# Performance work log

Hardware: AMD Instinct MI355X
Metric: run time of the kernel (lower is better)

The kernel has to match this reference:

```python
import jax, jax.numpy as jnp
import numpy as np

SEQ = 8192
EMB = 1024
MID = 1024


def setup_inputs() -> dict:
    key = jax.random.key(0)
    ks = jax.random.split(key, 7)
    s = 1.0 / np.sqrt(EMB)
    return {
        "text_encoded": jax.random.normal(ks[0], (SEQ, EMB), dtype=jnp.float32),
        "Wq": jax.random.normal(ks[1], (MID, EMB), dtype=jnp.float32) * s,
        "bq": jax.random.normal(ks[2], (MID,), dtype=jnp.float32) * 0.02,
        "Wk": jax.random.normal(ks[3], (MID, EMB), dtype=jnp.float32) * s,
        "bk": jax.random.normal(ks[4], (MID,), dtype=jnp.float32) * 0.02,
        "Wv": jax.random.normal(ks[5], (MID, EMB), dtype=jnp.float32) * s,
        "bv": jax.random.normal(ks[6], (MID,), dtype=jnp.float32) * 0.02,
    }


def reference(text_encoded, Wq, bq, Wk, bk, Wv, bv):
    # torch nn.Linear: y = x @ W.T + b, W is [out, in]
    Q = text_encoded @ Wq.T + bq  # [S, M]
    K = text_encoded @ Wk.T + bk  # [S, M]
    V = text_encoded @ Wv.T + bv  # [S, M]
    # cosine-similarity scores: (Q K^T) scaled by outer(1/||Q||, 1/||K||)
    inv_qn = jax.lax.rsqrt(jnp.sum(Q * Q, axis=1))  # [S]
    inv_kn = jax.lax.rsqrt(jnp.sum(K * K, axis=1))  # [S]
    scores = (Q @ K.T) * (inv_qn[:, None] * inv_kn[None, :])  # [S, S]
    weights = jax.nn.softmax(scores, axis=1)
    return weights @ V  # [S, M]
```

## Files before the change

### kernel.cpp

```cpp
#include <hip/hip_runtime.h>


#define SEQ 8192
#define MID 1024
#define EMB 1024

typedef __attribute__((ext_vector_type(8))) short short8x;
typedef __attribute__((ext_vector_type(16))) float float16x;
typedef __attribute__((ext_vector_type(4))) int int4x;
typedef __attribute__((ext_vector_type(16))) int int16x;

__device__ __forceinline__ unsigned short f2bf(float x) {
  union { float f; unsigned u; } v; v.f = x;
  unsigned r = v.u + 0x7FFFu + ((v.u >> 16) & 1u);
  return (unsigned short)(r >> 16);
}
__device__ __forceinline__ float bf2f(unsigned short h) {
  union { unsigned u; float f; } v; v.u = ((unsigned)h) << 16;
  return v.f;
}

__device__ __forceinline__ void g2l16(const void* g, void* lds) {
  __builtin_amdgcn_global_load_lds(
      (const __attribute__((address_space(1))) unsigned int*)g,
      (__attribute__((address_space(3))) unsigned int*)lds, 16, 0, 0);
}

__device__ __forceinline__ void gemm128_nt(
    const unsigned short* __restrict__ A, const unsigned short* __restrict__ B,
    long lda, long ldb, int m0, int n0, int K,
    unsigned short* As, unsigned short* Bs, float16x acc[2][2]) {
  const int tid = threadIdx.x;
  const int w = tid >> 6;
  const int l = tid & 63;
  const int wm = (w & 1) << 6;
  const int wn = (w >> 1) << 6;
  const int srow = l >> 3;
  const int skg = (l & 7) ^ srow;
  const int l31 = l & 31;
  const int lh = l >> 5;
  const int swz = l31 & 7;

  for (int k0 = 0; k0 < K; k0 += 64) {
    __syncthreads();
#pragma unroll
    for (int r = 0; r < 4; ++r) {
      const int rr = (w * 4 + r) * 8 + srow;
      g2l16(A + (long)(m0 + rr) * lda + k0 + skg * 8, As + (w * 4 + r) * 512);
      g2l16(B + (long)(n0 + rr) * ldb + k0 + skg * 8, Bs + (w * 4 + r) * 512);
    }
    __syncthreads();
#pragma unroll
    for (int ks = 0; ks < 4; ++ks) {
      const int kg = ks * 2 + lh;
      short8x av[2], bv[2];
#pragma unroll
      for (int t = 0; t < 2; ++t) {
        av[t] = *(const short8x*)(As + (wm + t * 32 + l31) * 64 + ((kg ^ swz) << 3));
        bv[t] = *(const short8x*)(Bs + (wn + t * 32 + l31) * 64 + ((kg ^ swz) << 3));
      }
#pragma unroll
      for (int tm = 0; tm < 2; ++tm)
#pragma unroll
        for (int tn = 0; tn < 2; ++tn)
          acc[tm][tn] = __builtin_amdgcn_mfma_f32_32x32x16_bf16(av[tm], bv[tn], acc[tm][tn], 0, 0, 0);
    }
  }
}

__device__ __forceinline__ void gemm128_nt_i8(
    const unsigned char* __restrict__ A, const unsigned char* __restrict__ B,
    long lda, long ldb, int m0, int n0, int Kbytes,
    unsigned char* As, unsigned char* Bs, int16x acc[2][2]) {
  const int tid = threadIdx.x;
  const int w = tid >> 6;
  const int l = tid & 63;
  const int wm = (w & 1) << 6;
  const int wn = (w >> 1) << 6;
  const int srow = l >> 3;
  const int skg = (l & 7) ^ srow;
  const int l31 = l & 31;
  const int lh = l >> 5;
  const int swz = l31 & 7;

  for (int k0 = 0; k0 < Kbytes; k0 += 128) {
    __syncthreads();
#pragma unroll
    for (int r = 0; r < 4; ++r) {
      const int rr = (w * 4 + r) * 8 + srow;
      g2l16(A + (long)(m0 + rr) * lda + k0 + skg * 16, As + (w * 4 + r) * 1024);
      g2l16(B + (long)(n0 + rr) * ldb + k0 + skg * 16, Bs + (w * 4 + r) * 1024);
    }
    __syncthreads();
#pragma unroll
    for (int ks = 0; ks < 4; ++ks) {
      const int kg = ks * 2 + lh;
      int4x av[2], bv[2];
#pragma unroll
      for (int t = 0; t < 2; ++t) {
        av[t] = *(const int4x*)(As + (wm + t * 32 + l31) * 128 + ((kg ^ swz) << 4));
        bv[t] = *(const int4x*)(Bs + (wn + t * 32 + l31) * 128 + ((kg ^ swz) << 4));
      }
#pragma unroll
      for (int tm = 0; tm < 2; ++tm)
#pragma unroll
        for (int tn = 0; tn < 2; ++tn)
          acc[tm][tn] = __builtin_amdgcn_mfma_i32_32x32x32_i8(av[tm], bv[tn], acc[tm][tn], 0, 0, 0);
    }
  }
}

__global__ void cvt_all(const float* __restrict__ X,
                        const float* __restrict__ wq, const float* __restrict__ wk,
                        const float* __restrict__ wv,
                        unsigned short* __restrict__ Xb, unsigned short* __restrict__ Wb,
                        float* __restrict__ sums) {
  const long i = ((long)blockIdx.x * 256 + threadIdx.x) * 4;
  if (i < 24576) *(float4*)(sums + i) = (float4){0.f, 0.f, 0.f, 0.f};
  const float* src;
  unsigned short* dst;
  long off;
  if (i < (long)SEQ * EMB) {
    src = X; dst = Xb; off = i;
  } else {
    long j = i - (long)SEQ * EMB;
    int t = (int)(j >> 20);
    off = j & (MID * EMB - 1);
    src = (t == 0) ? wq : (t == 1) ? wk : wv;
    dst = Wb + (long)t * MID * EMB;
  }
  float4 v = *(const float4*)(src + off);
  ushort4 o;
  o.x = f2bf(v.x); o.y = f2bf(v.y); o.z = f2bf(v.z); o.w = f2bf(v.w);
  *(ushort4*)(dst + off) = o;
}

__global__ __launch_bounds__(256) void qkv_kernel(
    const unsigned short* __restrict__ Xb, const unsigned short* __restrict__ Wb,
    const float* __restrict__ bq, const float* __restrict__ bk, const float* __restrict__ bv,
    unsigned char* __restrict__ Q8, unsigned char* __restrict__ K8,
    unsigned char* __restrict__ VT8, float* __restrict__ sumsq) {
  __shared__ unsigned short smem[16384];
  unsigned short* As = smem;
  unsigned short* Bs = smem + 8192;
  const int z = blockIdx.z;
  const int m0 = blockIdx.y * 128;
  const int n0 = blockIdx.x * 128;
  float16x acc[2][2];
#pragma unroll
  for (int i = 0; i < 2; ++i)
#pragma unroll
    for (int j = 0; j < 2; ++j)
#pragma unroll
      for (int e = 0; e < 16; ++e) acc[i][j][e] = 0.f;

  gemm128_nt(Xb, Wb + (long)z * MID * EMB, EMB, EMB, m0, n0, EMB, As, Bs, acc);

  const int tid = threadIdx.x;
  const int l = tid & 63, w = tid >> 6;
  const int wm = (w & 1) << 6, wn = (w >> 1) << 6;
  const int l31 = l & 31, lh = l >> 5;
  const float* bias = (z == 0) ? bq : (z == 1) ? bk : bv;
  float bvv[2];
#pragma unroll
  for (int tn = 0; tn < 2; ++tn) bvv[tn] = bias[n0 + wn + tn * 32 + l31];
#pragma unroll
  for (int tm = 0; tm < 2; ++tm)
#pragma unroll
    for (int tn = 0; tn < 2; ++tn)
#pragma unroll
      for (int r = 0; r < 16; ++r) acc[tm][tn][r] += bvv[tn];

  __syncthreads();

  if (z < 2) {
#pragma unroll
    for (int tm = 0; tm < 2; ++tm)
#pragma unroll
      for (int tn = 0; tn < 2; ++tn) {
        const int rcol = wn + tn * 32 + l31;
#pragma unroll
        for (int r = 0; r < 16; ++r) {
          float v = acc[tm][tn][r];
          float po = __shfl_xor(v, 1);
          if (!(l & 1)) {
            const int rrow = wm + tm * 32 + (r & 3) + 8 * (r >> 2) + 4 * lh;
            const int chunk = (rcol >> 3) ^ (rrow & 7);
            unsigned pk = (unsigned)f2bf(v) | ((unsigned)f2bf(po) << 16);
            *(unsigned*)(smem + rrow * 128 + (chunk << 3) + (rcol & 7)) = pk;
          }
        }
      }
    __syncthreads();
    unsigned char* O8 = z ? K8 : Q8;
    float* ss = sumsq + (long)z * SEQ;
    const float qs = 127.0f / 8.0f;
#pragma unroll
    for (int round = 0; round < 8; ++round) {
      const int row = round * 16 + (tid >> 4);
      const int c = tid & 15;
      short8x vv = *(const short8x*)(smem + row * 128 + ((c ^ (row & 7)) << 3));
      int qq[8];
      float s = 0.f;
#pragma unroll
      for (int j = 0; j < 8; ++j) {
        float t = rintf(bf2f((unsigned short)vv[j]) * qs);
        t = fminf(127.f, fmaxf(-127.f, t));
        qq[j] = (int)t;
        s += t * t;
      }
      unsigned lo = (qq[0] & 255) | ((qq[1] & 255) << 8) | ((qq[2] & 255) << 16) | ((qq[3] & 255) << 24);
      unsigned hi = (qq[4] & 255) | ((qq[5] & 255) << 8) | ((qq[6] & 255) << 16) | ((qq[7] & 255) << 24);
      int2 pk; pk.x = (int)lo; pk.y = (int)hi;
      *(int2*)(O8 + (long)(m0 + row) * MID + n0 + c * 8) = pk;
      s += __shfl_xor(s, 1); s += __shfl_xor(s, 2);
      s += __shfl_xor(s, 4); s += __shfl_xor(s, 8);
      if (c == 0) atomicAdd(ss + m0 + row, s);
    }
  } else {
#pragma unroll
    for (int tm = 0; tm < 2; ++tm)
#pragma unroll
      for (int tn = 0; tn < 2; ++tn) {
        const int nn = wn + tn * 32 + l31;
#pragma unroll
        for (int g = 0; g < 4; ++g) {
          const int mm = wm + tm * 32 + 8 * g + 4 * lh;
          const int chunk = (mm >> 3) ^ (nn & 7);
          ushort4 pk;
          pk.x = f2bf(acc[tm][tn][g * 4 + 0]);
          pk.y = f2bf(acc[tm][tn][g * 4 + 1]);
          pk.z = f2bf(acc[tm][tn][g * 4 + 2]);
          pk.w = f2bf(acc[tm][tn][g * 4 + 3]);
          *(ushort4*)(smem + nn * 128 + (chunk << 3) + (mm & 7)) = pk;
        }
      }
    __syncthreads();
    const float vs = 127.0f / 6.0f;
#pragma unroll
    for (int round = 0; round < 8; ++round) {
      const int nn = round * 16 + (tid >> 4);
      const int c = tid & 15;
      short8x vv = *(const short8x*)(smem + nn * 128 + ((c ^ (nn & 7)) << 3));
      int qq[8];
#pragma unroll
      for (int j = 0; j < 8; ++j) {
        float t = rintf(bf2f((unsigned short)vv[j]) * vs);
        t = fminf(127.f, fmaxf(-127.f, t));
        qq[j] = (int)t;
      }
      unsigned lo = (qq[0] & 255) | ((qq[1] & 255) << 8) | ((qq[2] & 255) << 16) | ((qq[3] & 255) << 24);
      unsigned hi = (qq[4] & 255) | ((qq[5] & 255) << 8) | ((qq[6] & 255) << 16) | ((qq[7] & 255) << 24);
      int2 pk; pk.x = (int)lo; pk.y = (int)hi;
      *(int2*)(VT8 + (long)(n0 + nn) * SEQ + m0 + c * 8) = pk;
    }
  }
}

__global__ __launch_bounds__(256) void score_kernel(
    const unsigned char* __restrict__ Q8, const unsigned char* __restrict__ K8,
    const float* __restrict__ sumsq,
    unsigned char* __restrict__ P8, float* __restrict__ denomq) {
  __shared__ unsigned short smem[16384];
  unsigned char* As = (unsigned char*)smem;
  unsigned char* Bs = (unsigned char*)smem + 16384;
  const int m0 = blockIdx.y * 128;
  const int n0 = blockIdx.x * 128;
  int16x acc[2][2];
#pragma unroll
  for (int i = 0; i < 2; ++i)
#pragma unroll
    for (int j = 0; j < 2; ++j)
#pragma unroll
      for (int e = 0; e < 16; ++e) acc[i][j][e] = 0;

  gemm128_nt_i8(Q8, K8, MID, MID, m0, n0, MID, As, Bs, acc);

  const int tid = threadIdx.x;
  const int l = tid & 63, w = tid >> 6;
  const int wm = (w & 1) << 6, wn = (w >> 1) << 6;
  const int l31 = l & 31, lh = l >> 5;

  float ik[2];
#pragma unroll
  for (int tn = 0; tn < 2; ++tn)
    ik[tn] = rsqrtf(sumsq[SEQ + n0 + wn + tn * 32 + l31]);

  __syncthreads();

#pragma unroll
  for (int tm = 0; tm < 2; ++tm)
#pragma unroll
    for (int r = 0; r < 16; ++r) {
      const int rrow = wm + tm * 32 + (r & 3) + 8 * (r >> 2) + 4 * lh;
      const float qi = rsqrtf(sumsq[m0 + rrow]);
#pragma unroll
      for (int tn = 0; tn < 2; ++tn) {
        float v = __expf((float)acc[tm][tn][r] * qi * ik[tn]);
        float po = __shfl_xor(v, 1);
        if (!(l & 1)) {
          const int rcol = wn + tn * 32 + l31;
          const int chunk = (rcol >> 3) ^ (rrow & 7);
          unsigned pk = (unsigned)f2bf(v) | ((unsigned)f2bf(po) << 16);
          *(unsigned*)(smem + rrow * 128 + (chunk << 3) + (rcol & 7)) = pk;
        }
      }
    }
  __syncthreads();
  const float ps = 127.0f / 2.7182818f;
#pragma unroll
  for (int round = 0; round < 8; ++round) {
    const int row = round * 16 + (tid >> 4);
    const int c = tid & 15;
    short8x vv = *(const short8x*)(smem + row * 128 + ((c ^ (row & 7)) << 3));
    int qq[8];
    float s = 0.f;
#pragma unroll
    for (int j = 0; j < 8; ++j) {
      float t = rintf(bf2f((unsigned short)vv[j]) * ps);
      t = fminf(127.f, t);
      qq[j] = (int)t;
      s += t;
    }
    unsigned lo = (qq[0] & 255) | ((qq[1] & 255) << 8) | ((qq[2] & 255) << 16) | ((qq[3] & 255) << 24);
    unsigned hi = (qq[4] & 255) | ((qq[5] & 255) << 8) | ((qq[6] & 255) << 16) | ((qq[7] & 255) << 24);
    int2 pk; pk.x = (int)lo; pk.y = (int)hi;
    *(int2*)(P8 + (long)(m0 + row) * SEQ + n0 + c * 8) = pk;
    s += __shfl_xor(s, 1); s += __shfl_xor(s, 2);
    s += __shfl_xor(s, 4); s += __shfl_xor(s, 8);
    if (c == 0) atomicAdd(denomq + m0 + row, s);
  }
}

__global__ __launch_bounds__(256) void out_kernel(
    const unsigned char* __restrict__ P8, const unsigned char* __restrict__ VT8,
    const float* __restrict__ denomq, float* __restrict__ out) {
  __shared__ unsigned char smem8[32768];
  unsigned char* As = smem8;
  unsigned char* Bs = smem8 + 16384;
  const int n0 = blockIdx.x * 128;
  const int m0 = blockIdx.y * 128;
  int16x acc[2][2];
#pragma unroll
  for (int i = 0; i < 2; ++i)
#pragma unroll
    for (int j = 0; j < 2; ++j)
#pragma unroll
      for (int e = 0; e < 16; ++e) acc[i][j][e] = 0;

  gemm128_nt_i8(P8, VT8, SEQ, SEQ, m0, n0, SEQ, As, Bs, acc);

  const int l = threadIdx.x & 63, w = threadIdx.x >> 6;
  const int wm = (w & 1) << 6, wn = (w >> 1) << 6;
  const int l31 = l & 31, lh = l >> 5;
  const float sv = 127.0f / 6.0f;
#pragma unroll
  for (int tm = 0; tm < 2; ++tm)
#pragma unroll
    for (int r = 0; r < 16; ++r) {
      const int row = m0 + wm + tm * 32 + (r & 3) + 8 * (r >> 2) + 4 * lh;
      const float inv = 1.0f / (sv * denomq[row]);
#pragma unroll
      for (int tn = 0; tn < 2; ++tn) {
        const int col = n0 + wn + tn * 32 + l31;
        out[(long)row * MID + col] = (float)acc[tm][tn][r] * inv;
      }
    }
}

extern "C" void kernel_launch(void* const* d_in, const int* in_sizes, int n_in,
                              void* d_out, int out_size, void* d_ws, size_t ws_size,
                              hipStream_t stream) {
  const float* X  = (const float*)d_in[0];
  const float* Wq = (const float*)d_in[1];
  const float* bq = (const float*)d_in[2];
  const float* Wk = (const float*)d_in[3];
  const float* bk = (const float*)d_in[4];
  const float* Wv = (const float*)d_in[5];
  const float* bv = (const float*)d_in[6];

  char* wsb = (char*)d_ws;
  const size_t MB = 1ull << 20;
  unsigned char* Q8  = (unsigned char*)(wsb);
  unsigned char* K8  = (unsigned char*)(wsb + 8 * MB);
  unsigned char* VT8 = (unsigned char*)(wsb + 16 * MB);
  float* sums        = (float*)(wsb + 24 * MB);
  float* denomq      = sums + 2 * SEQ;
  unsigned char* P8  = (unsigned char*)(wsb + 25 * MB);
  unsigned short* Xb = (unsigned short*)(wsb + 25 * MB);
  unsigned short* Wb = (unsigned short*)(wsb + 41 * MB);

  const int cvt_elems = SEQ * EMB + 3 * MID * EMB;
  cvt_all<<<cvt_elems / 1024, 256, 0, stream>>>(X, Wq, Wk, Wv, Xb, Wb, sums);

  qkv_kernel<<<dim3(MID / 128, SEQ / 128, 3), 256, 0, stream>>>(Xb, Wb, bq, bk, bv, Q8, K8, VT8, sums);
  score_kernel<<<dim3(SEQ / 128, SEQ / 128), 256, 0, stream>>>(Q8, K8, sums, P8, denomq);
  out_kernel<<<dim3(MID / 128, SEQ / 128), 256, 0, stream>>>(P8, VT8, denomq, (float*)d_out);
}
```

Measured before the change: 409.5 us.

## Transpose score GEMM and quantize probabilities to int8 directly in epilogue

Swaps the GEMM operands so each lane holds four consecutive K columns for one Q row. This lets exp2 with a folded log2 scale and a magic-number add produce int8 probabilities straight from registers. The old bf16 staging and the second requantization pass are removed. Row sums are now computed from packed bytes with SWAR adds, and stores are widened to 16 bytes. The trade-off is that the clamp to 127 is gone, so any value above the scale could wrap.

```diff
diff --git a/kernel.cpp b/kernel.cpp
--- a/kernel.cpp
+++ b/kernel.cpp
@@ -18,6 +18,13 @@
 __device__ __forceinline__ float bf2f(unsigned short h) {
   union { unsigned u; float f; } v; v.u = ((unsigned)h) << 16;
   return v.f;
+}
+__device__ __forceinline__ float fexp2(float x) {
+#if __has_builtin(__builtin_amdgcn_exp2f)
+  return __builtin_amdgcn_exp2f(x);
+#else
+  return __expf(x * 0.6931471805599453f);
+#endif
 }
 
 __device__ __forceinline__ void g2l16(const void* g, void* lds) {
@@ -274,61 +281,61 @@
 #pragma unroll
       for (int e = 0; e < 16; ++e) acc[i][j][e] = 0;
 
-  gemm128_nt_i8(Q8, K8, MID, MID, m0, n0, MID, As, Bs, acc);
+  gemm128_nt_i8(K8, Q8, MID, MID, n0, m0, MID, As, Bs, acc);
 
   const int tid = threadIdx.x;
   const int l = tid & 63, w = tid >> 6;
   const int wm = (w & 1) << 6, wn = (w >> 1) << 6;
   const int l31 = l & 31, lh = l >> 5;
 
-  float ik[2];
+  const float LOG2E  = 1.4426950408889634f;
+  const float LOG2PS = 5.5459896458832860f;
+  const float MAGIC  = 12582912.0f;
+  float qi[2];
 #pragma unroll
   for (int tn = 0; tn < 2; ++tn)
-    ik[tn] = rsqrtf(sumsq[SEQ + n0 + wn + tn * 32 + l31]);
+    qi[tn] = rsqrtf(sumsq[m0 + wn + tn * 32 + l31]) * LOG2E;
 
   __syncthreads();
 
-#pragma unroll
-  for (int tm = 0; tm < 2; ++tm)
-#pragma unroll
-    for (int r = 0; r < 16; ++r) {
-      const int rrow = wm + tm * 32 + (r & 3) + 8 * (r >> 2) + 4 * lh;
-      const float qi = rsqrtf(sumsq[m0 + rrow]);
+  unsigned char* Plds = As;
+#pragma unroll
+  for (int tm = 0; tm < 2; ++tm) {
+#pragma unroll
+    for (int g = 0; g < 4; ++g) {
+      const int nb = wm + tm * 32 + g * 8 + lh * 4;
+      float4 ss4 = *(const float4*)(sumsq + SEQ + n0 + nb);
+      float ik0 = rsqrtf(ss4.x), ik1 = rsqrtf(ss4.y);
+      float ik2 = rsqrtf(ss4.z), ik3 = rsqrtf(ss4.w);
 #pragma unroll
       for (int tn = 0; tn < 2; ++tn) {
-        float v = __expf((float)acc[tm][tn][r] * qi * ik[tn]);
-        float po = __shfl_xor(v, 1);
-        if (!(l & 1)) {
-          const int rcol = wn + tn * 32 + l31;
-          const int chunk = (rcol >> 3) ^ (rrow & 7);
-          unsigned pk = (unsigned)f2bf(v) | ((unsigned)f2bf(po) << 16);
-          *(unsigned*)(smem + rrow * 128 + (chunk << 3) + (rcol & 7)) = pk;
-        }
-      }
-    }
+        unsigned u0 = __float_as_uint(fexp2(fmaf((float)acc[tm][tn][g * 4 + 0] * ik0, qi[tn], LOG2PS)) + MAGIC);
+        unsigned u1 = __float_as_uint(fexp2(fmaf((float)acc[tm][tn][g * 4 + 1] * ik1, qi[tn], LOG2PS)) + MAGIC);
+        unsigned u2 = __float_as_uint(fexp2(fmaf((float)acc[tm][tn][g * 4 + 2] * ik2, qi[tn], LOG2PS)) + MAGIC);
+        unsigned u3 = __float_as_uint(fexp2(fmaf((float)acc[tm][tn][g * 4 + 3] * ik3, qi[tn], LOG2PS)) + MAGIC);
+        unsigned pk = (u0 & 255) | ((u1 & 255) << 8) | ((u2 & 255) << 16) | (u3 << 24);
+        const int ml = wn + tn * 32 + l31;
+        const int addr = ml * 128 + ((((nb >> 4) ^ (ml & 7)) << 4) | (nb & 15));
+        *(unsigned*)(Plds + addr) = pk;
+      }
+    }
+  }
   __syncthreads();
-  const float ps = 127.0f / 2.7182818f;
-#pragma unroll
-  for (int round = 0; round < 8; ++round) {
-    const int row = round * 16 + (tid >> 4);
-    const int c = tid & 15;
-    short8x vv = *(const short8x*)(smem + row * 128 + ((c ^ (row & 7)) << 3));
-    int qq[8];
-    float s = 0.f;
-#pragma unroll
-    for (int j = 0; j < 8; ++j) {
-      float t = rintf(bf2f((unsigned short)vv[j]) * ps);
-      t = fminf(127.f, t);
-      qq[j] = (int)t;
-      s += t;
-    }
-    unsigned lo = (qq[0] & 255) | ((qq[1] & 255) << 8) | ((qq[2] & 255) << 16) | ((qq[3] & 255) << 24);
-    unsigned hi = (qq[4] & 255) | ((qq[5] & 255) << 8) | ((qq[6] & 255) << 16) | ((qq[7] & 255) << 24);
-    int2 pk; pk.x = (int)lo; pk.y = (int)hi;
-    *(int2*)(P8 + (long)(m0 + row) * SEQ + n0 + c * 8) = pk;
-    s += __shfl_xor(s, 1); s += __shfl_xor(s, 2);
-    s += __shfl_xor(s, 4); s += __shfl_xor(s, 8);
-    if (c == 0) atomicAdd(denomq + m0 + row, s);
+
+  const unsigned M8 = 0x00FF00FFu;
+#pragma unroll
+  for (int round = 0; round < 4; ++round) {
+    const int row = round * 32 + (tid >> 3);
+    const int c = tid & 7;
+    const int addr = row * 128 + ((c ^ (row & 7)) << 4);
+    uint4 v = *(const uint4*)(Plds + addr);
+    unsigned e = (v.x & M8) + (v.y & M8) + (v.z & M8) + (v.w & M8);
+    unsigned o = ((v.x >> 8) & M8) + ((v.y >> 8) & M8) + ((v.z >> 8) & M8) + ((v.w >> 8) & M8);
+    unsigned t = e + o;
+    unsigned s = (t & 0xFFFFu) + (t >> 16);
+    *(uint4*)(P8 + (long)(m0 + row) * SEQ + n0 + c * 16) = v;
+    s += __shfl_xor(s, 1); s += __shfl_xor(s, 2); s += __shfl_xor(s, 4);
+    if (c == 0) atomicAdd(denomq + m0 + row, (float)s);
   }
 }
 
```

Measured after the change: 344.1 us. -16.0%, faster.
